# Optimization experiments

Hardware: AMD Instinct MI355X
Metric: run time of the kernel (lower is better)

Reference implementation:

```python
import jax, jax.numpy as jnp
import numpy as np

B, S, D, H = 256, 512, 128, 256  # batch, seq_len, input_dim, hidden_dim


def setup_inputs() -> dict:
    key = jax.random.key(0)
    ks = jax.random.split(key, 7)
    scale = 1.0 / np.sqrt(H)
    return {
        "x": jax.random.normal(ks[0], (B, S, D), dtype=jnp.float32),
        # WU_e: Linear(2H + S -> S, bias=False)
        "W_ue": jax.random.uniform(ks[1], (S, 2 * H + S), dtype=jnp.float32, minval=-scale, maxval=scale),
        # v_e: Linear(S -> 1, bias=False)
        "v_e": jax.random.uniform(ks[2], (1, S), dtype=jnp.float32, minval=-scale, maxval=scale),
        # LSTM params (PyTorch layout: gates order i,f,g,o)
        "W_ih": jax.random.uniform(ks[3], (4 * H, D), dtype=jnp.float32, minval=-scale, maxval=scale),
        "W_hh": jax.random.uniform(ks[4], (4 * H, H), dtype=jnp.float32, minval=-scale, maxval=scale),
        "b_ih": jax.random.uniform(ks[5], (4 * H,), dtype=jnp.float32, minval=-scale, maxval=scale),
        "b_hh": jax.random.uniform(ks[6], (4 * H,), dtype=jnp.float32, minval=-scale, maxval=scale),
    }


def reference(x, W_ue, v_e, W_ih, W_hh, b_ih, b_hh):
    b = x.shape[0]
    hdim = W_hh.shape[1]
    # Split WU_e into the part acting on (h,c) and the part acting on x rows.
    W_h = W_ue[:, : 2 * hdim]          # [S, 2H]
    W_x = W_ue[:, 2 * hdim:]           # [S, S]
    xT = jnp.transpose(x, (0, 2, 1))   # [B, D, S]
    # x contribution to attention logits is the same every step -> precompute.
    proj_x = jnp.einsum("bds,os->bdo", xT, W_x)  # [B, D, S]
    v = v_e[0]                          # [S]
    xs = jnp.transpose(x, (1, 0, 2))    # [S, B, D]

    def step(carry, x_t):
        h, c = carry                                    # [B, H] each
        hs = jnp.concatenate([h, c], axis=-1)           # [B, 2H]
        proj_h = hs @ W_h.T                             # [B, S]
        t = jnp.tanh(proj_h[:, None, :] + proj_x)       # [B, D, S]
        E = jnp.einsum("bds,s->bd", t, v)               # [B, D]
        alpha = jax.nn.softmax(E, axis=1)               # [B, D]
        inp = x_t * alpha                               # [B, D]
        gates = inp @ W_ih.T + b_ih + h @ W_hh.T + b_hh # [B, 4H]
        i, f, g, o = jnp.split(gates, 4, axis=-1)
        i = jax.nn.sigmoid(i)
        f = jax.nn.sigmoid(f)
        g = jnp.tanh(g)
        o = jax.nn.sigmoid(o)
        c_new = f * c + i * g
        h_new = o * jnp.tanh(c_new)
        return (h_new, c_new), h_new

    h0 = jnp.zeros((b, hdim), dtype=x.dtype)
    c0 = jnp.zeros((b, hdim), dtype=x.dtype)
    _, x_encoded = jax.lax.scan(step, (h0, c0), xs)  # [S, B, H]
    return x_encoded
```

## Files before the change

kernel.cpp:

```cpp
#include <hip/hip_runtime.h>
#include <hip/hip_bf16.h>

typedef __attribute__((ext_vector_type(8))) short bf16x8;
typedef __attribute__((ext_vector_type(4))) float f32x4;

#define C2LE 2.8853900817779268f
#define LOG2E 1.4426950408889634f
#define AGENT __HIP_MEMORY_SCOPE_AGENT
#define RLX __ATOMIC_RELAXED

static __device__ __forceinline__ float blo(unsigned q) { return __uint_as_float(q << 16); }
static __device__ __forceinline__ float bhi(unsigned q) { return __uint_as_float(q & 0xFFFF0000u); }
static __device__ __forceinline__ float rterm(float arg) {
  return __builtin_amdgcn_rcpf(1.0f + __builtin_amdgcn_exp2f(arg));
}
static __device__ __forceinline__ float sigm(float x) {
  return __builtin_amdgcn_rcpf(1.0f + __builtin_amdgcn_exp2f(-x * LOG2E));
}
static __device__ __forceinline__ float tanhe(float x) {
  return fmaf(-2.0f, __builtin_amdgcn_rcpf(1.0f + __builtin_amdgcn_exp2f(x * C2LE)), 1.0f);
}
static __device__ __forceinline__ unsigned packhilo(float x) {
  __hip_bfloat16 h = __float2bfloat16(x);
  float r = x - __bfloat162float(h);
  __hip_bfloat16 l = __float2bfloat16(r);
  return (unsigned)__bfloat16_as_ushort(h) | ((unsigned)__bfloat16_as_ushort(l) << 16);
}
static __device__ __forceinline__ void mkfrags(uint4 q0, uint4 q1, bf16x8& hi, bf16x8& lo) {
  uint4 h, l;
  h.x = __builtin_amdgcn_perm(q0.y, q0.x, 0x05040100u);
  h.y = __builtin_amdgcn_perm(q0.w, q0.z, 0x05040100u);
  h.z = __builtin_amdgcn_perm(q1.y, q1.x, 0x05040100u);
  h.w = __builtin_amdgcn_perm(q1.w, q1.z, 0x05040100u);
  l.x = __builtin_amdgcn_perm(q0.y, q0.x, 0x07060302u);
  l.y = __builtin_amdgcn_perm(q0.w, q0.z, 0x07060302u);
  l.z = __builtin_amdgcn_perm(q1.y, q1.x, 0x07060302u);
  l.w = __builtin_amdgcn_perm(q1.w, q1.z, 0x07060302u);
  hi = *(bf16x8*)&h;
  lo = *(bf16x8*)&l;
}
static __device__ __forceinline__ int swz(int e) { return e ^ ((e >> 4) & 7); }

__global__ void k_pack_whB(const float* __restrict__ wue, __hip_bfloat16* __restrict__ wp) {
  for (int idx = blockIdx.x * blockDim.x + threadIdx.x; idx < 262144;
       idx += gridDim.x * blockDim.x) {
    int j = idx & 7, l = (idx >> 3) & 63, kap = (idx >> 9) & 15, nb = (idx >> 13) & 3,
        sl = idx >> 15;
    int o = sl * 64 + nb * 16 + (l & 15);
    int dim = kap * 32 + (l >> 4) * 8 + j;
    wp[idx] = __float2bfloat16(wue[o * 1024 + dim]);
  }
}
__global__ void k_pack_w3B(const float* __restrict__ wih, const float* __restrict__ whh,
                           __hip_bfloat16* __restrict__ wp) {
  for (int idx = blockIdx.x * blockDim.x + threadIdx.x; idx < 393216;
       idx += gridDim.x * blockDim.x) {
    int j = idx & 7, l = (idx >> 3) & 63;
    int ks = (idx >> 9) % 12, r = (idx >> 9) / 12;
    int nb = r & 7, sl = r >> 3;
    int n = nb * 16 + (l & 15);
    int g = (n >> 5) * 256 + sl * 32 + (n & 31);
    int k = ks * 32 + (l >> 4) * 8 + j;
    float v = (k < 128) ? wih[g * 128 + k] : whh[g * 256 + (k - 128)];
    wp[idx] = __float2bfloat16(v);
  }
}
__global__ void k_bsum(const float* __restrict__ bih, const float* __restrict__ bhh,
                       float* __restrict__ bs) {
  int idx = blockIdx.x * blockDim.x + threadIdx.x;
  if (idx < 1024) bs[idx] = bih[idx] + bhh[idx];
}
__global__ void k_wxt(const float* __restrict__ wue, float* __restrict__ wxt) {
  for (int idx = blockIdx.x * blockDim.x + threadIdx.x; idx < 512 * 512;
       idx += gridDim.x * blockDim.x) {
    int o = idx & 511, s = idx >> 9;
    wxt[idx] = wue[o * 1024 + 512 + s];
  }
}

__global__ __launch_bounds__(512) void k_projx(const float* __restrict__ x,
                                               const float* __restrict__ wxt,
                                               __hip_bfloat16* __restrict__ px2) {
  __shared__ alignas(16) float xsT[32][512];
  const int b = blockIdx.x;
  const int tid = threadIdx.x;
  for (int dt = 0; dt < 4; ++dt) {
    __syncthreads();
    const float4* xr = (const float4*)(x + ((size_t)b << 16) + (size_t)tid * 128 + dt * 32);
#pragma unroll
    for (int q = 0; q < 8; ++q) {
      float4 vx = xr[q];
      xsT[q * 4 + 0][tid] = vx.x;
      xsT[q * 4 + 1][tid] = vx.y;
      xsT[q * 4 + 2][tid] = vx.z;
      xsT[q * 4 + 3][tid] = vx.w;
    }
    __syncthreads();
    const int o = tid;
    float acc[32];
#pragma unroll
    for (int dd = 0; dd < 32; ++dd) acc[dd] = 0.f;
    for (int s4 = 0; s4 < 128; ++s4) {
      float w0 = wxt[(s4 * 4 + 0) * 512 + o];
      float w1 = wxt[(s4 * 4 + 1) * 512 + o];
      float w2 = wxt[(s4 * 4 + 2) * 512 + o];
      float w3 = wxt[(s4 * 4 + 3) * 512 + o];
#pragma unroll
      for (int dd = 0; dd < 32; ++dd) {
        float4 xv = *(const float4*)&xsT[dd][s4 * 4];
        acc[dd] = fmaf(w0, xv.x, fmaf(w1, xv.y, fmaf(w2, xv.z, fmaf(w3, xv.w, acc[dd]))));
      }
    }
    for (int dd = 0; dd < 32; ++dd) {
      px2[((size_t)b * 128 + dt * 32 + dd) * 512 + o] = __float2bfloat16(acc[dd] * C2LE);
    }
  }
}

__global__ __launch_bounds__(1024) void k_main(
    const __hip_bfloat16* __restrict__ px2, const __hip_bfloat16* __restrict__ whB,
    const __hip_bfloat16* __restrict__ w3B, const float* __restrict__ bsum,
    const float* __restrict__ x, const float* __restrict__ ve,
    unsigned* __restrict__ hG, float* __restrict__ Eg, unsigned* __restrict__ ctrs,
    float* __restrict__ out) {
  __shared__ alignas(16) __hip_bfloat16 w3_l[49152];
  __shared__ alignas(16) uint4 hA0[1024];
  __shared__ alignas(16) uint4 hA1[1024];
  __shared__ alignas(16) uint4 uA0[256];
  __shared__ alignas(16) uint4 uA1[256];
  __shared__ float PHp[4][8][64];
  __shared__ float PH[512];
  __shared__ float gp[2][128][9];
  __shared__ float c_l[32][8];
  __shared__ float v_l[64];
  __shared__ float bs_l[128];
  __shared__ float zpart[16];
  __shared__ float vss_sh;

  const int grp = blockIdx.x & 31;
  const int sl = blockIdx.x >> 5;
  const int tid = threadIdx.x;
  const int lane = tid & 63;
  const int w = tid >> 6;
  const int b = tid >> 7;
  const int d = tid & 127;
  const int bG = grp * 8 + b;

  {
    const uint4* src = (const uint4*)(w3B + (size_t)sl * 49152);
    uint4* dst = (uint4*)w3_l;
    for (int i = tid; i < 6144; i += 1024) dst[i] = src[i];
  }
  bf16x8 whr[4];
  {
    const bf16x8* src =
        (const bf16x8*)whB + ((size_t)(sl * 4 + (w & 3)) * 16 + (w >> 2) * 4) * 64 + lane;
#pragma unroll
    for (int i = 0; i < 4; ++i) whr[i] = src[i * 64];
  }
  uint4 pxr[8];
  {
    const uint4* p4 = (const uint4*)(px2 + ((size_t)bG * 128 + d) * 512 + sl * 64);
#pragma unroll
    for (int i = 0; i < 8; ++i) pxr[i] = p4[i];
  }
  if (tid < 64) v_l[tid] = ve[sl * 64 + tid];
  if (tid < 128) bs_l[tid] = bsum[(tid >> 5) * 256 + sl * 32 + (tid & 31)];
  if (tid < 256) c_l[tid >> 3][tid & 7] = 0.f;
  {
    uint4 z = {0, 0, 0, 0};
    hA0[tid] = z;
    hA1[tid] = z;
    if (tid < 256) {
      uA0[tid] = z;
      uA1[tid] = z;
    }
  }
  if (tid == 0) {
    float s = 0.f;
    for (int i = 0; i < 64; ++i) s += ve[sl * 64 + i];
    vss_sh = s;
  }
  __syncthreads();
  const float vss = vss_sh;
  unsigned* ctrA = ctrs + grp * 64;
  unsigned* ctrB = ctrA + 32;
  float xv = x[((size_t)bG * 512) * 128 + d];

  for (int t = 0; t < 512; ++t) {
    const int par = t & 1;

    {
      const unsigned long long* hp =
          (const unsigned long long*)(hG + (size_t)(par * 32 + grp) * 4096) + tid * 2;
      unsigned long long a0 = __hip_atomic_load(hp, RLX, AGENT);
      unsigned long long a1 = __hip_atomic_load(hp + 1, RLX, AGENT);
      int p = tid * 4;
      int e = ((p >> 6) << 4) + ((p >> 3) & 7);
      int ep = swz(e);
      uint4 q;
      q.x = (unsigned)a0;
      q.y = (unsigned)(a0 >> 32);
      q.z = (unsigned)a1;
      q.w = (unsigned)(a1 >> 32);
      if (p & 4) hA1[ep] = q;
      else hA0[ep] = q;
    }
    if (tid < 128)
      __hip_atomic_store(Eg + (size_t)((1 - par) * 32 + grp) * 1024 + sl * 128 + tid, 0.f, RLX,
                         AGENT);
    __syncthreads();

    {
      const int kq = w >> 2, nb = w & 3;
      f32x4 acc = {0.f, 0.f, 0.f, 0.f};
#pragma unroll
      for (int i = 0; i < 4; ++i) {
        int ep = swz((kq * 4 + i) * 64 + lane);
        uint4 q0 = hA0[ep], q1 = hA1[ep];
        bf16x8 ahi, alo;
        mkfrags(q0, q1, ahi, alo);
        acc = __builtin_amdgcn_mfma_f32_16x16x32_bf16(ahi, whr[i], acc, 0, 0, 0);
        acc = __builtin_amdgcn_mfma_f32_16x16x32_bf16(alo, whr[i], acc, 0, 0, 0);
      }
      if (lane < 32) {
        int r16 = lane >> 4, c16 = lane & 15;
#pragma unroll
        for (int rr = 0; rr < 4; ++rr) PHp[kq][r16 * 4 + rr][nb * 16 + c16] = acc[rr];
      }
    }
    __syncthreads();
    if (tid < 512)
      PH[tid] = (PHp[0][tid >> 6][tid & 63] + PHp[1][tid >> 6][tid & 63] +
                 PHp[2][tid >> 6][tid & 63] + PHp[3][tid >> 6][tid & 63]) *
                C2LE;
    __syncthreads();

    {
      float R = 0.f;
      const float* PHb = &PH[b * 64];
#pragma unroll 2
      for (int s8 = 0; s8 < 8; ++s8) {
        uint4 q = pxr[s8];
        float4 pa = *(const float4*)&PHb[s8 * 8];
        float4 pb = *(const float4*)&PHb[s8 * 8 + 4];
        float4 va = *(const float4*)&v_l[s8 * 8];
        float4 vb = *(const float4*)&v_l[s8 * 8 + 4];
        R = fmaf(va.x, rterm(pa.x + blo(q.x)), R);
        R = fmaf(va.y, rterm(pa.y + bhi(q.x)), R);
        R = fmaf(va.z, rterm(pa.z + blo(q.y)), R);
        R = fmaf(va.w, rterm(pa.w + bhi(q.y)), R);
        R = fmaf(vb.x, rterm(pb.x + blo(q.z)), R);
        R = fmaf(vb.y, rterm(pb.y + bhi(q.z)), R);
        R = fmaf(vb.z, rterm(pb.z + blo(q.w)), R);
        R = fmaf(vb.w, rterm(pb.w + bhi(q.w)), R);
      }
      __hip_atomic_fetch_add(Eg + (size_t)(par * 32 + grp) * 1024 + b * 128 + d,
                             fmaf(-2.f, R, vss), RLX, AGENT);
    }

    const int nb3 = w & 7, kh3 = w >> 3;
    f32x4 acc3 = {0.f, 0.f, 0.f, 0.f};
#pragma unroll
    for (int i = 0; i < 4; ++i) {
      int ks = 4 + kh3 * 4 + i;
      int ep = swz((ks - 4) * 64 + lane);
      uint4 q0 = hA0[ep], q1 = hA1[ep];
      bf16x8 ahi, alo;
      mkfrags(q0, q1, ahi, alo);
      bf16x8 bf = ((const bf16x8*)w3_l)[((size_t)nb3 * 12 + ks) * 64 + lane];
      acc3 = __builtin_amdgcn_mfma_f32_16x16x32_bf16(ahi, bf, acc3, 0, 0, 0);
      acc3 = __builtin_amdgcn_mfma_f32_16x16x32_bf16(alo, bf, acc3, 0, 0, 0);
    }
    __syncthreads();
    if (tid == 0) {
      __hip_atomic_fetch_add(ctrA, 1u, RLX, AGENT);
      while (__hip_atomic_load(ctrA, RLX, AGENT) < 8u * (t + 1)) __builtin_amdgcn_s_sleep(1);
    }
    __syncthreads();

    float Ev = __hip_atomic_load(Eg + (size_t)(par * 32 + grp) * 1024 + b * 128 + d, RLX, AGENT);
    float e = __builtin_amdgcn_exp2f(Ev * LOG2E);
    {
      float z = e;
#pragma unroll
      for (int m = 1; m < 64; m <<= 1) z += __shfl_xor(z, m);
      if (lane == 0) zpart[w] = z;
    }
    __syncthreads();
    {
      float zf = zpart[2 * b] + zpart[2 * b + 1];
      float u = xv * e * __builtin_amdgcn_rcpf(zf);
      int ep = swz((d >> 5) * 64 + ((d >> 3) & 3) * 16 + b);
      unsigned* dst = (d & 4) ? (unsigned*)&uA1[ep] : (unsigned*)&uA0[ep];
      dst[d & 3] = packhilo(u);
    }
    __syncthreads();

#pragma unroll
    for (int i = 0; i < 2; ++i) {
      int ks = kh3 * 2 + i;
      int ep = swz(ks * 64 + lane);
      uint4 q0 = uA0[ep], q1 = uA1[ep];
      bf16x8 ahi, alo;
      mkfrags(q0, q1, ahi, alo);
      bf16x8 bf = ((const bf16x8*)w3_l)[((size_t)nb3 * 12 + ks) * 64 + lane];
      acc3 = __builtin_amdgcn_mfma_f32_16x16x32_bf16(ahi, bf, acc3, 0, 0, 0);
      acc3 = __builtin_amdgcn_mfma_f32_16x16x32_bf16(alo, bf, acc3, 0, 0, 0);
    }
    if (lane < 32) {
      int r16 = lane >> 4, c16 = lane & 15;
#pragma unroll
      for (int rr = 0; rr < 4; ++rr) gp[kh3][nb3 * 16 + c16][r16 * 4 + rr] = acc3[rr];
    }
    __syncthreads();

    float h_new;
    if (tid < 256) {
      int bb = tid & 7, jj = tid >> 3;
      float gi = gp[0][jj][bb] + gp[1][jj][bb] + bs_l[jj];
      float gf = gp[0][32 + jj][bb] + gp[1][32 + jj][bb] + bs_l[32 + jj];
      float gg = gp[0][64 + jj][bb] + gp[1][64 + jj][bb] + bs_l[64 + jj];
      float go = gp[0][96 + jj][bb] + gp[1][96 + jj][bb] + bs_l[96 + jj];
      float i_ = sigm(gi), f_ = sigm(gf), g_ = tanhe(gg), o_ = sigm(go);
      float c_new = fmaf(f_, c_l[jj][bb], i_ * g_);
      h_new = o_ * tanhe(c_new);
      c_l[jj][bb] = c_new;
      int dd = sl * 32 + jj;
      int p = (((dd >> 5) * 4 + ((dd >> 3) & 3)) * 8 + bb) * 8 + (dd & 7);
      unsigned* hw = hG + (size_t)((1 - par) * 32 + grp) * 4096;
      __hip_atomic_store(hw + p, packhilo(h_new), RLX, AGENT);
      __hip_atomic_store(hw + p + 2048, packhilo(c_new), RLX, AGENT);
    }
    __syncthreads();
    if (tid == 0) __hip_atomic_fetch_add(ctrB, 1u, RLX, AGENT);
    if (tid < 256) {
      int bb = tid & 7, jj = tid >> 3;
      __builtin_nontemporal_store(h_new,
                                  out + ((size_t)t * 256 + grp * 8 + bb) * 256 + sl * 32 + jj);
    }
    int tn = (t < 511) ? t + 1 : 511;
    float xv_n = x[((size_t)bG * 512 + tn) * 128 + d];
    if (tid == 0) {
      while (__hip_atomic_load(ctrB, RLX, AGENT) < 8u * (t + 1)) __builtin_amdgcn_s_sleep(1);
    }
    __syncthreads();
    xv = xv_n;
  }
}

extern "C" void kernel_launch(void* const* d_in, const int* in_sizes, int n_in,
                              void* d_out, int out_size, void* d_ws, size_t ws_size,
                              hipStream_t stream) {
  const float* x = (const float*)d_in[0];
  const float* wue = (const float*)d_in[1];
  const float* ve = (const float*)d_in[2];
  const float* wih = (const float*)d_in[3];
  const float* whh = (const float*)d_in[4];
  const float* bih = (const float*)d_in[5];
  const float* bhh = (const float*)d_in[6];
  float* out = (float*)d_out;

  char* ws = (char*)d_ws;
  __hip_bfloat16* px2 = (__hip_bfloat16*)(ws);
  __hip_bfloat16* whB = (__hip_bfloat16*)(ws + 33554432);
  __hip_bfloat16* w3B = (__hip_bfloat16*)(ws + 34078720);
  float* bsum = (float*)(ws + 34865152);
  float* Eg = (float*)(ws + 34869248);
  unsigned* ctrs = (unsigned*)(ws + 35131392);
  unsigned* hG = (unsigned*)(ws + 35139584);
  float* wxt = (float*)(ws + 36188160);

  k_pack_whB<<<1024, 256, 0, stream>>>(wue, whB);
  k_pack_w3B<<<1024, 256, 0, stream>>>(wih, whh, w3B);
  k_bsum<<<4, 256, 0, stream>>>(bih, bhh, bsum);
  k_wxt<<<256, 256, 0, stream>>>(wue, wxt);
  k_projx<<<256, 512, 0, stream>>>(x, wxt, px2);
  hipMemsetAsync(hG, 0, 1048576, stream);
  hipMemsetAsync(Eg, 0, 262144, stream);
  hipMemsetAsync(ctrs, 0, 8192, stream);
  k_main<<<256, 1024, 0, stream>>>(px2, whB, w3B, bsum, x, ve, hG, Eg, ctrs, out);
}
```

Before: 4.916 ms.

## Split recurrent LSTM-attention work over 512 blocks, reading gate weights from global

Each 8-batch group is now split across 16 hidden-dimension slices instead of 8, so the persistent kernel launches 512 blocks and each block does half the per-step MFMA and elementwise work. The weight-packing kernels and all per-slice indexing, partial-sum reductions and barrier counter thresholds are rewritten to match. The LDS copy of the gate weight matrix is removed, and gate weights are read from global memory on every step. The intent is to shorten the per-step critical path through more parallelism. In exchange it adds more participants in each cross-block spin barrier, extra L2 weight traffic, and needs two 1024-thread blocks resident per CU for the spin barriers to make progress.

```diff
diff --git a/kernel.cpp b/kernel.cpp
--- a/kernel.cpp
+++ b/kernel.cpp
@@ -44,9 +44,9 @@
 __global__ void k_pack_whB(const float* __restrict__ wue, __hip_bfloat16* __restrict__ wp) {
   for (int idx = blockIdx.x * blockDim.x + threadIdx.x; idx < 262144;
        idx += gridDim.x * blockDim.x) {
-    int j = idx & 7, l = (idx >> 3) & 63, kap = (idx >> 9) & 15, nb = (idx >> 13) & 3,
-        sl = idx >> 15;
-    int o = sl * 64 + nb * 16 + (l & 15);
+    int j = idx & 7, l = (idx >> 3) & 63, kap = (idx >> 9) & 15, nb = (idx >> 13) & 1,
+        sl = idx >> 14;
+    int o = sl * 32 + nb * 16 + (l & 15);
     int dim = kap * 32 + (l >> 4) * 8 + j;
     wp[idx] = __float2bfloat16(wue[o * 1024 + dim]);
   }
@@ -56,10 +56,10 @@
   for (int idx = blockIdx.x * blockDim.x + threadIdx.x; idx < 393216;
        idx += gridDim.x * blockDim.x) {
     int j = idx & 7, l = (idx >> 3) & 63;
-    int ks = (idx >> 9) % 12, r = (idx >> 9) / 12;
-    int nb = r & 7, sl = r >> 3;
-    int n = nb * 16 + (l & 15);
-    int g = (n >> 5) * 256 + sl * 32 + (n & 31);
+    int rest = idx >> 9;
+    int ks = rest % 12, r = rest / 12;
+    int ty = r & 3, sl = r >> 2;
+    int g = ty * 256 + sl * 16 + (l & 15);
     int k = ks * 32 + (l >> 4) * 8 + j;
     float v = (k < 128) ? wih[g * 128 + k] : whh[g * 256 + (k - 128)];
     wp[idx] = __float2bfloat16(v);
@@ -117,23 +117,22 @@
   }
 }
 
-__global__ __launch_bounds__(1024) void k_main(
+__global__ __launch_bounds__(1024, 8) void k_main(
     const __hip_bfloat16* __restrict__ px2, const __hip_bfloat16* __restrict__ whB,
     const __hip_bfloat16* __restrict__ w3B, const float* __restrict__ bsum,
     const float* __restrict__ x, const float* __restrict__ ve,
     unsigned* __restrict__ hG, float* __restrict__ Eg, unsigned* __restrict__ ctrs,
     float* __restrict__ out) {
-  __shared__ alignas(16) __hip_bfloat16 w3_l[49152];
   __shared__ alignas(16) uint4 hA0[1024];
   __shared__ alignas(16) uint4 hA1[1024];
   __shared__ alignas(16) uint4 uA0[256];
   __shared__ alignas(16) uint4 uA1[256];
-  __shared__ float PHp[4][8][64];
-  __shared__ float PH[512];
-  __shared__ float gp[2][128][9];
-  __shared__ float c_l[32][8];
-  __shared__ float v_l[64];
-  __shared__ float bs_l[128];
+  __shared__ float PHp[8][8][32];
+  __shared__ float PH[256];
+  __shared__ float gp[4][64][9];
+  __shared__ float c_l[16][8];
+  __shared__ float v_l[32];
+  __shared__ float bs_l[64];
   __shared__ float zpart[16];
   __shared__ float vss_sh;
 
@@ -146,27 +145,22 @@
   const int d = tid & 127;
   const int bG = grp * 8 + b;
 
+  bf16x8 whr[2];
   {
-    const uint4* src = (const uint4*)(w3B + (size_t)sl * 49152);
-    uint4* dst = (uint4*)w3_l;
-    for (int i = tid; i < 6144; i += 1024) dst[i] = src[i];
-  }
-  bf16x8 whr[4];
+    const int nb = w & 1, kq = w >> 1;
+    const bf16x8* src = (const bf16x8*)whB + ((size_t)(sl * 2 + nb) * 16 + kq * 2) * 64 + lane;
+    whr[0] = src[0];
+    whr[1] = src[64];
+  }
+  uint4 pxr[4];
   {
-    const bf16x8* src =
-        (const bf16x8*)whB + ((size_t)(sl * 4 + (w & 3)) * 16 + (w >> 2) * 4) * 64 + lane;
-#pragma unroll
-    for (int i = 0; i < 4; ++i) whr[i] = src[i * 64];
-  }
-  uint4 pxr[8];
-  {
-    const uint4* p4 = (const uint4*)(px2 + ((size_t)bG * 128 + d) * 512 + sl * 64);
-#pragma unroll
-    for (int i = 0; i < 8; ++i) pxr[i] = p4[i];
-  }
-  if (tid < 64) v_l[tid] = ve[sl * 64 + tid];
-  if (tid < 128) bs_l[tid] = bsum[(tid >> 5) * 256 + sl * 32 + (tid & 31)];
-  if (tid < 256) c_l[tid >> 3][tid & 7] = 0.f;
+    const uint4* p4 = (const uint4*)(px2 + ((size_t)bG * 128 + d) * 512 + sl * 32);
+#pragma unroll
+    for (int i = 0; i < 4; ++i) pxr[i] = p4[i];
+  }
+  if (tid < 32) v_l[tid] = ve[sl * 32 + tid];
+  if (tid < 64) bs_l[tid] = bsum[(tid >> 4) * 256 + sl * 16 + (tid & 15)];
+  if (tid < 128) c_l[tid >> 3][tid & 7] = 0.f;
   {
     uint4 z = {0, 0, 0, 0};
     hA0[tid] = z;
@@ -178,7 +172,7 @@
   }
   if (tid == 0) {
     float s = 0.f;
-    for (int i = 0; i < 64; ++i) s += ve[sl * 64 + i];
+    for (int i = 0; i < 32; ++i) s += ve[sl * 32 + i];
     vss_sh = s;
   }
   __syncthreads();
@@ -206,17 +200,17 @@
       if (p & 4) hA1[ep] = q;
       else hA0[ep] = q;
     }
-    if (tid < 128)
-      __hip_atomic_store(Eg + (size_t)((1 - par) * 32 + grp) * 1024 + sl * 128 + tid, 0.f, RLX,
+    if (tid < 64)
+      __hip_atomic_store(Eg + (size_t)((1 - par) * 32 + grp) * 1024 + sl * 64 + tid, 0.f, RLX,
                          AGENT);
     __syncthreads();
 
     {
-      const int kq = w >> 2, nb = w & 3;
+      const int kq = w >> 1, nb = w & 1;
       f32x4 acc = {0.f, 0.f, 0.f, 0.f};
 #pragma unroll
-      for (int i = 0; i < 4; ++i) {
-        int ep = swz((kq * 4 + i) * 64 + lane);
+      for (int i = 0; i < 2; ++i) {
+        int ep = swz((kq * 2 + i) * 64 + lane);
         uint4 q0 = hA0[ep], q1 = hA1[ep];
         bf16x8 ahi, alo;
         mkfrags(q0, q1, ahi, alo);
@@ -230,17 +224,19 @@
       }
     }
     __syncthreads();
-    if (tid < 512)
-      PH[tid] = (PHp[0][tid >> 6][tid & 63] + PHp[1][tid >> 6][tid & 63] +
-                 PHp[2][tid >> 6][tid & 63] + PHp[3][tid >> 6][tid & 63]) *
-                C2LE;
+    if (tid < 256) {
+      int bb = tid >> 5, o = tid & 31;
+      float s = ((PHp[0][bb][o] + PHp[1][bb][o]) + (PHp[2][bb][o] + PHp[3][bb][o])) +
+                ((PHp[4][bb][o] + PHp[5][bb][o]) + (PHp[6][bb][o] + PHp[7][bb][o]));
+      PH[tid] = s * C2LE;
+    }
     __syncthreads();
 
     {
       float R = 0.f;
-      const float* PHb = &PH[b * 64];
-#pragma unroll 2
-      for (int s8 = 0; s8 < 8; ++s8) {
+      const float* PHb = &PH[b * 32];
+#pragma unroll
+      for (int s8 = 0; s8 < 4; ++s8) {
         uint4 q = pxr[s8];
         float4 pa = *(const float4*)&PHb[s8 * 8];
         float4 pb = *(const float4*)&PHb[s8 * 8 + 4];
@@ -259,23 +255,23 @@
                              fmaf(-2.f, R, vss), RLX, AGENT);
     }
 
-    const int nb3 = w & 7, kh3 = w >> 3;
+    const int ty3 = w & 3, kh3 = w >> 2;
     f32x4 acc3 = {0.f, 0.f, 0.f, 0.f};
 #pragma unroll
-    for (int i = 0; i < 4; ++i) {
-      int ks = 4 + kh3 * 4 + i;
+    for (int i = 0; i < 2; ++i) {
+      int ks = 4 + kh3 * 2 + i;
       int ep = swz((ks - 4) * 64 + lane);
       uint4 q0 = hA0[ep], q1 = hA1[ep];
       bf16x8 ahi, alo;
       mkfrags(q0, q1, ahi, alo);
-      bf16x8 bf = ((const bf16x8*)w3_l)[((size_t)nb3 * 12 + ks) * 64 + lane];
+      bf16x8 bf = ((const bf16x8*)w3B)[(((size_t)sl * 4 + ty3) * 12 + ks) * 64 + lane];
       acc3 = __builtin_amdgcn_mfma_f32_16x16x32_bf16(ahi, bf, acc3, 0, 0, 0);
       acc3 = __builtin_amdgcn_mfma_f32_16x16x32_bf16(alo, bf, acc3, 0, 0, 0);
     }
     __syncthreads();
     if (tid == 0) {
       __hip_atomic_fetch_add(ctrA, 1u, RLX, AGENT);
-      while (__hip_atomic_load(ctrA, RLX, AGENT) < 8u * (t + 1)) __builtin_amdgcn_s_sleep(1);
+      while (__hip_atomic_load(ctrA, RLX, AGENT) < 16u * (t + 1)) __builtin_amdgcn_s_sleep(1);
     }
     __syncthreads();
 
@@ -297,36 +293,38 @@
     }
     __syncthreads();
 
-#pragma unroll
-    for (int i = 0; i < 2; ++i) {
-      int ks = kh3 * 2 + i;
+    {
+      int ks = kh3;
       int ep = swz(ks * 64 + lane);
       uint4 q0 = uA0[ep], q1 = uA1[ep];
       bf16x8 ahi, alo;
       mkfrags(q0, q1, ahi, alo);
-      bf16x8 bf = ((const bf16x8*)w3_l)[((size_t)nb3 * 12 + ks) * 64 + lane];
+      bf16x8 bf = ((const bf16x8*)w3B)[(((size_t)sl * 4 + ty3) * 12 + ks) * 64 + lane];
       acc3 = __builtin_amdgcn_mfma_f32_16x16x32_bf16(ahi, bf, acc3, 0, 0, 0);
       acc3 = __builtin_amdgcn_mfma_f32_16x16x32_bf16(alo, bf, acc3, 0, 0, 0);
     }
     if (lane < 32) {
       int r16 = lane >> 4, c16 = lane & 15;
 #pragma unroll
-      for (int rr = 0; rr < 4; ++rr) gp[kh3][nb3 * 16 + c16][r16 * 4 + rr] = acc3[rr];
+      for (int rr = 0; rr < 4; ++rr) gp[kh3][ty3 * 16 + c16][r16 * 4 + rr] = acc3[rr];
     }
     __syncthreads();
 
     float h_new;
-    if (tid < 256) {
+    if (tid < 128) {
       int bb = tid & 7, jj = tid >> 3;
-      float gi = gp[0][jj][bb] + gp[1][jj][bb] + bs_l[jj];
-      float gf = gp[0][32 + jj][bb] + gp[1][32 + jj][bb] + bs_l[32 + jj];
-      float gg = gp[0][64 + jj][bb] + gp[1][64 + jj][bb] + bs_l[64 + jj];
-      float go = gp[0][96 + jj][bb] + gp[1][96 + jj][bb] + bs_l[96 + jj];
+      float gi = gp[0][jj][bb] + gp[1][jj][bb] + gp[2][jj][bb] + gp[3][jj][bb] + bs_l[jj];
+      float gf = gp[0][16 + jj][bb] + gp[1][16 + jj][bb] + gp[2][16 + jj][bb] +
+                 gp[3][16 + jj][bb] + bs_l[16 + jj];
+      float gg = gp[0][32 + jj][bb] + gp[1][32 + jj][bb] + gp[2][32 + jj][bb] +
+                 gp[3][32 + jj][bb] + bs_l[32 + jj];
+      float go = gp[0][48 + jj][bb] + gp[1][48 + jj][bb] + gp[2][48 + jj][bb] +
+                 gp[3][48 + jj][bb] + bs_l[48 + jj];
       float i_ = sigm(gi), f_ = sigm(gf), g_ = tanhe(gg), o_ = sigm(go);
       float c_new = fmaf(f_, c_l[jj][bb], i_ * g_);
       h_new = o_ * tanhe(c_new);
       c_l[jj][bb] = c_new;
-      int dd = sl * 32 + jj;
+      int dd = sl * 16 + jj;
       int p = (((dd >> 5) * 4 + ((dd >> 3) & 3)) * 8 + bb) * 8 + (dd & 7);
       unsigned* hw = hG + (size_t)((1 - par) * 32 + grp) * 4096;
       __hip_atomic_store(hw + p, packhilo(h_new), RLX, AGENT);
@@ -334,15 +332,15 @@
     }
     __syncthreads();
     if (tid == 0) __hip_atomic_fetch_add(ctrB, 1u, RLX, AGENT);
-    if (tid < 256) {
+    if (tid < 128) {
       int bb = tid & 7, jj = tid >> 3;
       __builtin_nontemporal_store(h_new,
-                                  out + ((size_t)t * 256 + grp * 8 + bb) * 256 + sl * 32 + jj);
+                                  out + ((size_t)t * 256 + grp * 8 + bb) * 256 + sl * 16 + jj);
     }
     int tn = (t < 511) ? t + 1 : 511;
     float xv_n = x[((size_t)bG * 512 + tn) * 128 + d];
     if (tid == 0) {
-      while (__hip_atomic_load(ctrB, RLX, AGENT) < 8u * (t + 1)) __builtin_amdgcn_s_sleep(1);
+      while (__hip_atomic_load(ctrB, RLX, AGENT) < 16u * (t + 1)) __builtin_amdgcn_s_sleep(1);
     }
     __syncthreads();
     xv = xv_n;
@@ -379,5 +377,5 @@
   hipMemsetAsync(hG, 0, 1048576, stream);
   hipMemsetAsync(Eg, 0, 262144, stream);
   hipMemsetAsync(ctrs, 0, 8192, stream);
-  k_main<<<256, 1024, 0, stream>>>(px2, whB, w3B, bsum, x, ve, hG, Eg, ctrs, out);
-}
+  k_main<<<512, 1024, 0, stream>>>(px2, whB, w3B, bsum, x, ve, hG, Eg, ctrs, out);
+}
```

After: 9.397 ms. 1.91x slower.
